# Kernel optimization log

Hardware: AMD Instinct MI355X
Metric: run time of the kernel (lower is better)

## Reference

```python
import jax, jax.numpy as jnp
import numpy as np

D = 128                # state dim d; full ODE state is d + d*d (x and flattened W)
T = 4096               # number of saved timesteps

# Tsit5 Butcher tableau (Tsitouras 2011), 5th-order solution weights = a7 row (b7 = 0, FSAL)
A21 = 0.161
A31, A32 = -0.008480655492356989, 0.335480655492357
A41, A42, A43 = 2.8971530571054935, -6.359448489975075, 4.3622954328695815
A51, A52, A53, A54 = 5.325864828439257, -11.748883564062828, 7.4955393428898365, -0.09249506636175525
A61, A62, A63, A64, A65 = 5.86145544294642, -12.92096931784711, 8.159367898576159, -0.071584973281401, -0.028269050394068383
B1, B2, B3, B4, B5, B6 = 0.09646076681806523, 0.01, 0.4798896504144996, 1.379008574103742, -3.290069515436081, 2.324710524099774

def _vf(y, Bm):
    # Func.__call__: x = y[:d]; W = reshape(y[d:], (d,d)); f = DynX(W@x) = W@x; bw = W @ b(W) = W @ Bm
    x = y[:D]
    W = y[D:].reshape(D, D)
    return jnp.concatenate([W @ x, (W @ Bm).reshape(D * D)])

def _tsit5_step(y, dt, Bm):
    k1 = _vf(y, Bm)
    k2 = _vf(y + dt * (A21 * k1), Bm)
    k3 = _vf(y + dt * (A31 * k1 + A32 * k2), Bm)
    k4 = _vf(y + dt * (A41 * k1 + A42 * k2 + A43 * k3), Bm)
    k5 = _vf(y + dt * (A51 * k1 + A52 * k2 + A53 * k3 + A54 * k4), Bm)
    k6 = _vf(y + dt * (A61 * k1 + A62 * k2 + A63 * k3 + A64 * k4 + A65 * k5), Bm)
    return y + dt * (B1 * k1 + B2 * k2 + B3 * k3 + B4 * k4 + B5 * k5 + B6 * k6)

def setup_inputs() -> dict:
    key = jax.random.key(0)
    k1, k2 = jax.random.split(key)
    ts = jnp.arange(T, dtype=jnp.float32) / (T - 1)          # save times in [0, 1]
    y0 = 0.1 * jax.random.normal(k1, (D + D * D,), dtype=jnp.float32)
    B = 0.02 * jax.random.normal(k2, (D, D), dtype=jnp.float32)  # WeightDynamics: b(W) = B
    return {"ts": ts, "y0": y0, "B": B}

def reference(ts, y0, B):
    # One Tsit5 step per save interval (deterministic fixed-step counterpart of
    # diffrax.diffeqsolve(ODETerm(func), Tsit5(), saveat=SaveAt(ts=ts))).
    dts = ts[1:] - ts[:-1]
    def step(y, dt):
        y_new = _tsit5_step(y, dt, B)
        return y_new, y_new
    _, ys_rest = jax.lax.scan(step, y0, dts)
    return jnp.concatenate([y0[None], ys_rest], axis=0)  # [T, D + D*D]
```

## Files before the change

### kernel.cpp

```cpp
#include <hip/hip_runtime.h>
#include <cstring>

#define D 128
#define ROW 16512
#define DTF (1.0f/4095.0f)
#define HSTEP (64.0f/4095.0f)
#define H4F  (256.0f/4095.0f)
#define LDA 132
#define LDB 132
#define NV  5

#define XCP_OFF 4096
#define MAT_OFF 12416

#define S_ZT      3
#define S_V(m)    (4+(m))
#define S_AT(J)   (11+(J))
#define S_BMT(J)  (27+(J))
#define S_PT      42
#define S_GT      57

struct __align__(16) F4 { float v[4]; };
typedef float f4v __attribute__((ext_vector_type(4)));

__device__ __forceinline__ float* slotp(float* ws, int k){ return ws + MAT_OFF + (size_t)k*16384; }
__device__ __forceinline__ const float* slotpc(const float* ws, int k){ return ws + MAT_OFF + (size_t)k*16384; }

struct CFX { float cf[64][5]; float cx[64][5]; };
struct CMB { float c[31][7]; };
struct EK  { double e[4][4]; };

__device__ __forceinline__ void ldA(const float* A, int r0, float (*As)[LDA]) {
  const F4* A4 = (const F4*)(A + (size_t)r0*128);
  for (int q = threadIdx.x; q < 512; q += 256) {
    F4 x = A4[q];
    *(F4*)&As[q>>5][(q&31)<<2] = x;
  }
}
__device__ __forceinline__ void mmcT(const float (*As)[LDA], const float (*Bs)[LDB], F4& o0, F4& o1) {
  const int rl = threadIdx.x >> 5, c0 = (threadIdx.x & 31) << 2;
  F4 a0s, a1s;
  #pragma unroll
  for (int e = 0; e < 4; ++e) { a0s.v[e] = 0.f; a1s.v[e] = 0.f; }
  #pragma unroll 8
  for (int k = 0; k < 128; ++k) {
    const F4 bv = *(const F4*)&Bs[k][c0];
    const float a0 = As[rl][k], a1 = As[rl+8][k];
    #pragma unroll
    for (int e = 0; e < 4; ++e) {
      a0s.v[e] = fmaf(a0, bv.v[e], a0s.v[e]);
      a1s.v[e] = fmaf(a1, bv.v[e], a1s.v[e]);
    }
  }
  o0 = a0s; o1 = a1s;
}

__global__ __launch_bounds__(256) void k_vchain(const float* y0, const float* Bm,
                                                float* ws, float* out, CMB cmb) {
  __shared__ float As[16][LDA];
  __shared__ float Bs[128][LDB];
  int b = blockIdx.x, t = threadIdx.x;
  const float* W0 = y0 + D;
  const int rl = t >> 5, c0 = (t & 31) << 2;
  if (b < 32) {
    int m = (b >> 3) + 1, strip = b & 7;
    const F4* B4 = (const F4*)Bm;
    for (int q = t; q < 4096; q += 256) {
      F4 x = B4[q]; F4 o;
      #pragma unroll
      for (int e = 0; e < 4; ++e) o.v[e] = HSTEP * x.v[e];
      *(F4*)&Bs[q>>5][(q&31)<<2] = o;
    }
    ldA(W0, strip*16, As);
    __syncthreads();
    F4 o0, o1;
    for (int p = 0; p < m; ++p) {
      mmcT(As, Bs, o0, o1);
      if (p+1 < m) {
        __syncthreads();
        *(F4*)&As[rl][c0] = o0;
        *(F4*)&As[rl+8][c0] = o1;
        __syncthreads();
      }
    }
    float* Vp = slotp(ws, S_V(m));
    *(F4*)&Vp[(size_t)(strip*16+rl)*128 + c0]   = o0;
    *(F4*)&Vp[(size_t)(strip*16+rl+8)*128 + c0] = o1;
  } else if (b < 36) {
    int base = (b-32)*1024;
    for (int i = 0; i < 4; ++i) {
      int q = base + t + i*256;
      ((F4*)out)[q] = ((const F4*)y0)[q];
    }
  } else if (b == 36) {
    if (t < 128) { out[16384+t] = y0[16384+t]; ws[XCP_OFF+t] = y0[t]; }
  } else if (b < 41) {
    int base = (b-37)*1024;
    F4* Vp = (F4*)slotp(ws, S_V(0));
    for (int i = 0; i < 4; ++i) { int q = base + t + i*256; Vp[q] = ((const F4*)W0)[q]; }
  } else if (b < 45) {
    int base = (b-41)*1024;
    float* ZT = slotp(ws, S_ZT);
    for (int i = 0; i < 4; ++i) {
      int q = base + t + i*256;
      F4 x = ((const F4*)Bm)[q];
      int r = q>>5, cc2 = (q&31)<<2;
      #pragma unroll
      for (int e = 0; e < 4; ++e) ZT[(size_t)(cc2+e)*128 + r] = HSTEP * x.v[e];
    }
  } else {
    int idx = b - 45;
    int mat = idx >> 3, strip = idx & 7;
    int slot = (mat < 16) ? S_AT(mat) : S_BMT(mat-16);
    const float* cc = cmb.c[mat];
    const F4* B4 = (const F4*)Bm;
    for (int q = t; q < 4096; q += 256) {
      F4 x = B4[q]; F4 o;
      #pragma unroll
      for (int e = 0; e < 4; ++e) o.v[e] = HSTEP * x.v[e];
      *(F4*)&Bs[q>>5][(q&31)<<2] = o;
    }
    const F4 s0 = *(const F4*)&W0[(size_t)(strip*16+rl)*128 + c0];
    const F4 s1 = *(const F4*)&W0[(size_t)(strip*16+rl+8)*128 + c0];
    F4 t0, t1;
    #pragma unroll
    for (int e = 0; e < 4; ++e) { t0.v[e] = cc[6]*s0.v[e]; t1.v[e] = cc[6]*s1.v[e]; }
    *(F4*)&As[rl][c0] = t0; *(F4*)&As[rl+8][c0] = t1;
    __syncthreads();
    F4 o0, o1;
    for (int k = 5; k >= 0; --k) {
      mmcT(As, Bs, o0, o1);
      #pragma unroll
      for (int e = 0; e < 4; ++e) { o0.v[e] += cc[k]*s0.v[e]; o1.v[e] += cc[k]*s1.v[e]; }
      if (k > 0) {
        __syncthreads();
        *(F4*)&As[rl][c0] = o0; *(F4*)&As[rl+8][c0] = o1;
        __syncthreads();
      }
    }
    float* Cp = slotp(ws, slot);
    int r0 = strip*16 + rl;
    #pragma unroll
    for (int e = 0; e < 4; ++e) {
      Cp[(size_t)(c0+e)*128 + r0]     = o0.v[e];
      Cp[(size_t)(c0+e)*128 + r0 + 8] = o1.v[e];
    }
  }
}

__global__ __launch_bounds__(256) void k_phiT(float* ws) {
  __shared__ float Bs1[128][LDB];
  __shared__ float Bs2[128][LDB];
  __shared__ float Aw[16][LDA];
  __shared__ float Asb[16][LDA];
  int J = blockIdx.x >> 3, strip = blockIdx.x & 7, t = threadIdx.x;
  const int rl = t >> 5, c0 = (t & 31) << 2;
  const float* a  = slotpc(ws, S_AT(J));
  const float* b  = slotpc(ws, S_BMT(J));
  const float* ap = slotpc(ws, S_AT(J+1));
  { const F4* s=(const F4*)b;  for (int q=t;q<4096;q+=256) *(F4*)&Bs1[q>>5][(q&31)<<2]=s[q]; }
  { const F4* s=(const F4*)ap; for (int q=t;q<4096;q+=256) *(F4*)&Bs2[q>>5][(q&31)<<2]=s[q]; }
  ldA(a, strip*16, Aw);
  ldA(b, strip*16, Asb);
  __syncthreads();
  F4 pa0, pa1;
  {
    const F4 p0 = *(const F4*)&ap[(size_t)(strip*16+rl)*128 + c0];
    const F4 p1 = *(const F4*)&ap[(size_t)(strip*16+rl+8)*128 + c0];
    #pragma unroll
    for (int e = 0; e < 4; ++e) {
      pa0.v[e] = Aw[rl][c0+e]   + 4.f*Asb[rl][c0+e]   + p0.v[e];
      pa1.v[e] = Aw[rl+8][c0+e] + 4.f*Asb[rl+8][c0+e] + p1.v[e];
    }
  }
  const float h = H4F, wh = h, wh2 = 0.5f*h*h, wh3 = 0.25f*h*h*h;
  F4 o0, o1;
  mmcT(Aw, Bs1, o0, o1);
  #pragma unroll
  for (int e = 0; e < 4; ++e) { pa0.v[e] += wh*o0.v[e]; pa1.v[e] += wh*o1.v[e]; }
  __syncthreads();
  *(F4*)&Aw[rl][c0] = o0; *(F4*)&Aw[rl+8][c0] = o1;
  __syncthreads();
  mmcT(Aw, Bs1, o0, o1);
  #pragma unroll
  for (int e = 0; e < 4; ++e) { pa0.v[e] += wh2*o0.v[e]; pa1.v[e] += wh2*o1.v[e]; }
  __syncthreads();
  *(F4*)&Aw[rl][c0] = o0; *(F4*)&Aw[rl+8][c0] = o1;
  __syncthreads();
  mmcT(Aw, Bs2, o0, o1);
  #pragma unroll
  for (int e = 0; e < 4; ++e) { pa0.v[e] += wh3*o0.v[e]; pa1.v[e] += wh3*o1.v[e]; }
  __syncthreads();
  mmcT(Asb, Bs1, o0, o1);
  #pragma unroll
  for (int e = 0; e < 4; ++e) { pa0.v[e] += wh*o0.v[e]; pa1.v[e] += wh*o1.v[e]; }
  *(F4*)&Aw[rl][c0] = o0; *(F4*)&Aw[rl+8][c0] = o1;
  __syncthreads();
  mmcT(Asb, Bs2, o0, o1);
  #pragma unroll
  for (int e = 0; e < 4; ++e) { pa0.v[e] += wh*o0.v[e]; pa1.v[e] += wh*o1.v[e]; }
  mmcT(Aw, Bs2, o0, o1);
  #pragma unroll
  for (int e = 0; e < 4; ++e) { pa0.v[e] += wh2*o0.v[e]; pa1.v[e] += wh2*o1.v[e]; }
  float* PT = slotp(ws, S_PT + J);
  const float h6 = h / 6.0f;
  #pragma unroll
  for (int half = 0; half < 2; ++half) {
    int r = strip*16 + rl + half*8;
    F4 pa = half ? pa1 : pa0;
    F4 o;
    #pragma unroll
    for (int e = 0; e < 4; ++e)
      o.v[e] = ((r == c0+e) ? 1.0f : 0.0f) + h6*pa.v[e];
    *(F4*)&PT[(size_t)r*128 + c0] = o;
  }
}

__global__ __launch_bounds__(256) void k_phiT2(float* ws) {
  __shared__ float As[16][LDA];
  __shared__ float Bs[128][LDB];
  int K = blockIdx.x >> 3, strip = blockIdx.x & 7, t = threadIdx.x;
  const int rl = t >> 5, c0 = (t & 31) << 2;
  ldA(slotpc(ws, S_PT + 4*K), strip*16, As);
  F4 o0, o1;
  for (int s = 1; s <= 3; ++s) {
    const F4* sd = (const F4*)slotpc(ws, S_PT + 4*K + s);
    for (int q = t; q < 4096; q += 256) *(F4*)&Bs[q>>5][(q&31)<<2] = sd[q];
    __syncthreads();
    mmcT(As, Bs, o0, o1);
    __syncthreads();
    if (s < 3) {
      *(F4*)&As[rl][c0] = o0; *(F4*)&As[rl+8][c0] = o1;
      __syncthreads();
    }
  }
  float* GT = slotp(ws, S_GT + K);
  *(F4*)&GT[(size_t)(strip*16+rl)*128 + c0]   = o0;
  *(F4*)&GT[(size_t)(strip*16+rl+8)*128 + c0] = o1;
}

__global__ __launch_bounds__(256, 2) void k_fused(float* ws, float* out, EK ek, CFX cfx) {
  __shared__ __align__(16) float smf[NV*4096];
  int t = threadIdx.x;

  if (blockIdx.x >= 64) {
    int bb = blockIdx.x - 64;
    int g = bb >> 2, qt = bb & 3;
    for (int m = 0; m < NV; ++m) {
      const F4* Vq = (const F4*)(slotpc(ws, S_V(m)) + qt*4096);
      F4* L = (F4*)&smf[m*4096];
      for (int q4 = t; q4 < 1024; q4 += 256) L[q4] = Vq[q4];
    }
    __syncthreads();
    for (int nn = 0; nn < 16; ++nn) {
      int n = g*16 + nn, j = n >> 6, i = n & 63;
      float c[5];
      #pragma unroll
      for (int p = 0; p < 5; ++p) {
        float s = 0.f;
        #pragma unroll
        for (int m = 0; m <= 4; ++m) {
          int qm = p - m;
          if (qm >= 0) s = fmaf(cfx.cf[i][m], cfx.cx[j][qm], s);
        }
        c[p] = s;
      }
      float* dst = out + (size_t)n*ROW + D + qt*4096;
      #pragma unroll
      for (int k = 0; k < 4; ++k) {
        int qq = k*256 + t;
        f4v o = {0.f, 0.f, 0.f, 0.f};
        #pragma unroll
        for (int m = 0; m < NV; ++m) {
          F4 v = *(const F4*)&smf[m*4096 + 4*qq];
          #pragma unroll
          for (int e = 0; e < 4; ++e) o[e] = fmaf(c[m], v.v[e], o[e]);
        }
        *(f4v*)(dst + 4*(size_t)qq) = o;
      }
    }
    return;
  }

  float* za   = smf;
  float* zb   = smf + 640;
  float* Pv   = smf + 1280;
  float* Qv   = smf + 1920;
  float* xv   = smf + 2560;
  float* kv   = smf + 2688;
  float* red  = smf + 2816;
  float* uv   = smf + 2944;
  float (*cfs)[5] = (float (*)[5])(smf + 3200);

  int J = blockIdx.x >> 2, w = blockIdx.x & 3;
  int r = t & 127, hh = t >> 7;
  if (t < 128) xv[t] = ws[XCP_OFF + t];
  if (t < 64) {
    double di = (double)(w*64 + t);
    double b1 = di, b2 = b1*(di-1.0)*0.5, b3 = b2*(di-2.0)*(1.0/3.0), b4 = b3*(di-3.0)*0.25;
    cfs[t][0] = 1.f;
    cfs[t][1] = (float)(b1*ek.e[0][0]);
    cfs[t][2] = (float)(b1*ek.e[0][1] + b2*ek.e[1][1]);
    cfs[t][3] = (float)(b1*ek.e[0][2] + b2*ek.e[1][2] + b3*ek.e[2][2]);
    cfs[t][4] = (float)(b1*ek.e[0][3] + b2*ek.e[1][3] + b3*ek.e[2][3] + b4*ek.e[3][3]);
  }
  __syncthreads();

  int a = J >> 2;
  for (int k = 0; k < a; ++k) {
    const float* PT = slotpc(ws, S_GT + k);
    float s = 0.f;
    #pragma unroll 8
    for (int c = hh*64; c < hh*64+64; ++c) s = fmaf(PT[(size_t)c*128 + r], xv[c], s);
    if (hh) red[r] = s;
    __syncthreads();
    if (!hh) xv[r] = s + red[r];
    __syncthreads();
  }
  for (int jj = a*4; jj < J; ++jj) {
    const float* PT = slotpc(ws, S_PT + jj);
    float s = 0.f;
    #pragma unroll 8
    for (int c = hh*64; c < hh*64+64; ++c) s = fmaf(PT[(size_t)c*128 + r], xv[c], s);
    if (hh) red[r] = s;
    __syncthreads();
    if (!hh) xv[r] = s + red[r];
    __syncthreads();
  }
  if (J > 0 && w == 0 && t < 128) out[(size_t)(256*J)*ROW + t] = xv[t];

  const float* ATJ = slotpc(ws, S_AT(J));
  {
    float s = 0.f;
    #pragma unroll 8
    for (int c = hh*64; c < hh*64 + 64; ++c) s = fmaf(ATJ[(size_t)c*128 + r], xv[c], s);
    if (hh) red[r] = s;
    __syncthreads();
    if (!hh) kv[r] = s + red[r];
    __syncthreads();
  }
  if (t < 128) { za[t] = xv[t]; zb[t] = kv[t]; }
  __syncthreads();
  const float* ZTg = slotpc(ws, S_ZT);
  for (int m = 1; m <= 4; ++m) {
    float sa = 0.f, sb = 0.f;
    #pragma unroll 8
    for (int c = hh*64; c < hh*64 + 64; ++c) {
      float zv = ZTg[(size_t)c*128 + r];
      sa = fmaf(zv, za[(m-1)*128 + c], sa);
      sb = fmaf(zv, zb[(m-1)*128 + c], sb);
    }
    if (hh) { red[r] = sa; uv[r] = sb; }
    __syncthreads();
    if (!hh) { za[m*128 + r] = sa + red[r]; zb[m*128 + r] = sb + uv[r]; }
    __syncthreads();
  }
  {
    float sa[5] = {0,0,0,0,0}, sb[5] = {0,0,0,0,0};
    #pragma unroll 8
    for (int c = hh*64; c < hh*64 + 64; ++c) {
      float av = ATJ[(size_t)c*128 + r];
      #pragma unroll
      for (int m = 0; m <= 4; ++m) {
        sa[m] = fmaf(av, za[m*128 + c], sa[m]);
        sb[m] = fmaf(av, zb[m*128 + c], sb[m]);
      }
    }
    #pragma unroll
    for (int m = 0; m <= 4; ++m) {
      if (hh) { red[r] = sa[m]; uv[r] = sb[m]; }
      __syncthreads();
      if (!hh) { Pv[m*128 + r] = sa[m] + red[r]; Qv[m*128 + r] = sb[m] + uv[r]; }
      __syncthreads();
    }
  }
  float xr = xv[r], kr = kv[r];
  #pragma unroll 4
  for (int l = 0; l < 32; ++l) {
    int il = 2*l + hh;
    int i = w*64 + il;
    if (i >= 1) {
      float hi = i * DTF;
      float k2r = 0.f;
      #pragma unroll
      for (int m = 0; m <= 4; ++m)
        k2r = fmaf(cfs[il][m], Pv[m*128 + r] + hi*Qv[m*128 + r], k2r);
      out[(size_t)(256*J + i)*ROW + r] = xr + 0.5f*hi*(kr + k2r);
    }
  }
}

static void pmul16(const double* a, const double* b, double* o) {
  double r[16];
  for (int i = 0; i < 16; ++i) r[i] = 0.0;
  for (int i = 0; i < 16; ++i) {
    double ai = a[i];
    if (ai == 0.0) continue;
    for (int k = 0; i + k < 16; ++k) r[i+k] += ai*b[k];
  }
  for (int i = 0; i < 16; ++i) o[i] = r[i];
}

extern "C" void kernel_launch(void* const* d_in, const int* in_sizes, int n_in,
                              void* d_out, int out_size, void* d_ws, size_t ws_size,
                              hipStream_t stream) {
  (void)in_sizes; (void)n_in; (void)out_size; (void)ws_size;
  const float* y0 = (const float*)d_in[1];
  const float* Bm = (const float*)d_in[2];
  float* out = (float*)d_out;
  float* ws  = (float*)d_ws;

  double At[7][7]; memset(At, 0, sizeof(At));
  At[2][1] = 0.161;
  At[3][1] = -0.008480655492356989; At[3][2] = 0.335480655492357;
  At[4][1] = 2.8971530571054935;  At[4][2] = -6.359448489975075;  At[4][3] = 4.3622954328695815;
  At[5][1] = 5.325864828439257;   At[5][2] = -11.748883564062828; At[5][3] = 7.4955393428898365;  At[5][4] = -0.09249506636175525;
  At[6][1] = 5.86145544294642;    At[6][2] = -12.92096931784711;  At[6][3] = 8.159367898576159;   At[6][4] = -0.071584973281401; At[6][5] = -0.028269050394068383;
  const double dB[7] = {0, 0.09646076681806523, 0.01, 0.4798896504144996,
                        1.379008574103742, -3.290069515436081, 2.324710524099774};
  double C[7][16]; memset(C, 0, sizeof(C));
  C[1][0] = 1.0;
  for (int s = 2; s <= 6; ++s) {
    C[s][0] = 1.0;
    for (int k = 1; k < 16; ++k) {
      double acc = 0.0;
      for (int l = 1; l < s; ++l) acc += At[s][l]*C[l][k-1];
      C[s][k] = acc;
    }
  }
  double M[16]; memset(M, 0, sizeof(M)); M[0] = 1.0;
  for (int k = 1; k < 16; ++k) {
    double acc = 0.0;
    for (int s = 1; s <= 6; ++s) acc += dB[s]*C[s][k-1];
    M[k] = acc;
  }
  double p64m[16]; p64m[0] = 1.0;
  for (int m = 1; m < 16; ++m) p64m[m] = p64m[m-1]*64.0;

  CFX cfx; memset(&cfx, 0, sizeof(cfx));
  CMB cmb; memset(&cmb, 0, sizeof(cmb));
  double cur[16]; memset(cur, 0, sizeof(cur)); cur[0] = 1.0;
  for (int n = 0; n <= 4032; ++n) {
    if (n < 64)  for (int m = 0; m <= 4; ++m) cfx.cf[n][m] = (float)(cur[m]/p64m[m]);
    if ((n & 63) == 0) {
      int j = n >> 6;
      if (j < 64) for (int m = 0; m <= 4; ++m) cfx.cx[j][m] = (float)(cur[m]/p64m[m]);
    }
    if ((n & 255) == 0) {
      int J = n >> 8;
      if (J <= 15) for (int m = 0; m <= 6; ++m) cmb.c[J][m] = (float)(cur[m]/p64m[m]);
    }
    if ((n & 255) == 128) {
      int J = (n - 128) >> 8;
      if (J <= 14) for (int m = 0; m <= 6; ++m) cmb.c[16+J][m] = (float)(cur[m]/p64m[m]);
    }
    pmul16(cur, M, cur);
  }

  EK ek; memset(&ek, 0, sizeof(ek));
  {
    double e1[5] = {0,0,0,0,0}, e2[5] = {0,0,0,0,0}, e3[5] = {0,0,0,0,0}, e4[5] = {0,0,0,0,0};
    for (int m = 1; m <= 4; ++m) e1[m] = M[m];
    for (int m = 2; m <= 4; ++m) for (int a = 1; a < m; ++a) e2[m] += e1[a]*e1[m-a];
    for (int m = 3; m <= 4; ++m) for (int a = 2; a < m; ++a) e3[m] += e2[a]*e1[m-a];
    e4[4] = e3[3]*e1[1];
    for (int m = 1; m <= 4; ++m) {
      ek.e[0][m-1] = e1[m]/p64m[m];
      ek.e[1][m-1] = e2[m]/p64m[m];
      ek.e[2][m-1] = e3[m]/p64m[m];
      ek.e[3][m-1] = e4[m]/p64m[m];
    }
  }

  k_vchain<<<293, 256, 0, stream>>>(y0, Bm, ws, out, cmb);
  k_phiT<<<120, 256, 0, stream>>>(ws);
  k_phiT2<<<24, 256, 0, stream>>>(ws);
  k_fused<<<1088, 256, 0, stream>>>(ws, out, ek, cfx);
}
```

Before: 134.6 us.

## Stream V basis from global memory in output blocks, shrink shared memory

The output-writing blocks of the fused kernel no longer stage the five V basis quarters (80 KB) in shared memory. They read them directly from global/L2 per float4, with a grid-stride mapping over 2048 blocks. Shared memory drops to about 14 KB and the 2-block launch bound is removed. This aims to raise occupancy and improve store streaming, at the cost of re-reading V from cache for every output row and recomputing coefficients per thread.

```diff
diff --git a/kernel.cpp b/kernel.cpp
--- a/kernel.cpp
+++ b/kernel.cpp
@@ -19,6 +19,8 @@
 #define S_BMT(J)  (27+(J))
 #define S_PT      42
 #define S_GT      57
+
+#define NFB 2048
 
 struct __align__(16) F4 { float v[4]; };
 typedef float f4v __attribute__((ext_vector_type(4)));
@@ -239,21 +241,20 @@
   *(F4*)&GT[(size_t)(strip*16+rl+8)*128 + c0] = o1;
 }
 
-__global__ __launch_bounds__(256, 2) void k_fused(float* ws, float* out, EK ek, CFX cfx) {
-  __shared__ __align__(16) float smf[NV*4096];
+__global__ __launch_bounds__(256) void k_fused(float* ws, float* out, EK ek, CFX cfx) {
+  __shared__ __align__(16) float smf[3520];
   int t = threadIdx.x;
 
   if (blockIdx.x >= 64) {
-    int bb = blockIdx.x - 64;
-    int g = bb >> 2, qt = bb & 3;
-    for (int m = 0; m < NV; ++m) {
-      const F4* Vq = (const F4*)(slotpc(ws, S_V(m)) + qt*4096);
-      F4* L = (F4*)&smf[m*4096];
-      for (int q4 = t; q4 < 1024; q4 += 256) L[q4] = Vq[q4];
-    }
-    __syncthreads();
-    for (int nn = 0; nn < 16; ++nn) {
-      int n = g*16 + nn, j = n >> 6, i = n & 63;
+    int fb = blockIdx.x - 64;
+    const F4* Vg[NV];
+    #pragma unroll
+    for (int m = 0; m < NV; ++m) Vg[m] = (const F4*)slotpc(ws, S_V(m));
+    for (int it = 0; it < 32; ++it) {
+      int f = (it*NFB + fb)*256 + t;
+      int n = f >> 12;
+      int q4 = f & 4095;
+      int j = n >> 6, i = n & 63;
       float c[5];
       #pragma unroll
       for (int p = 0; p < 5; ++p) {
@@ -265,19 +266,14 @@
         }
         c[p] = s;
       }
-      float* dst = out + (size_t)n*ROW + D + qt*4096;
-      #pragma unroll
-      for (int k = 0; k < 4; ++k) {
-        int qq = k*256 + t;
-        f4v o = {0.f, 0.f, 0.f, 0.f};
+      f4v o = {0.f, 0.f, 0.f, 0.f};
+      #pragma unroll
+      for (int m = 0; m < NV; ++m) {
+        F4 v = Vg[m][q4];
         #pragma unroll
-        for (int m = 0; m < NV; ++m) {
-          F4 v = *(const F4*)&smf[m*4096 + 4*qq];
-          #pragma unroll
-          for (int e = 0; e < 4; ++e) o[e] = fmaf(c[m], v.v[e], o[e]);
-        }
-        *(f4v*)(dst + 4*(size_t)qq) = o;
+        for (int e = 0; e < 4; ++e) o[e] = fmaf(c[m], v.v[e], o[e]);
       }
+      *(f4v*)(out + (size_t)n*ROW + D + 4*(size_t)q4) = o;
     }
     return;
   }
@@ -475,5 +471,5 @@
   k_vchain<<<293, 256, 0, stream>>>(y0, Bm, ws, out, cmb);
   k_phiT<<<120, 256, 0, stream>>>(ws);
   k_phiT2<<<24, 256, 0, stream>>>(ws);
-  k_fused<<<1088, 256, 0, stream>>>(ws, out, ek, cfx);
-}
+  k_fused<<<64 + NFB, 256, 0, stream>>>(ws, out, ek, cfx);
+}
```

Result: slower. 153.6 us (+14.2%).
